# Kernel tuning notes

Hardware: AMD Instinct MI355X
Metric: run time of the kernel (lower is better)

Reference implementation:

```python
import jax, jax.numpy as jnp
import numpy as np

MAX_DEG = 3
DEG_DIMS = [1, 3, 5, 7]          # degree_to_dim(d) = 2d+1
SUM_DIM = 16                     # sum of DEG_DIMS
FREQ_SUM = 44                    # sum over (d_in,d_out) of 2*min(d_in,d_out)+1
C = 32                           # channels per degree (in == out, FULL fusion)
EDGE_DIM = 2                     # fiber_edge[0] + 1
MID = 32                         # RadialProfile mid_dim
E = 4096
N = 1024


def setup_inputs() -> dict:
    key = jax.random.key(0)
    ks = jax.random.split(key, 16)
    inp = {}
    for d, dim in enumerate(DEG_DIMS):
        inp[f"node_feats_{d}"] = jax.random.normal(ks[d], (N, C, dim), jnp.float32)
    inp["edge_feats_0"] = jax.random.normal(ks[4], (E, EDGE_DIM, 1), jnp.float32)
    inp["basis"] = jax.random.normal(ks[5], (E, SUM_DIM, FREQ_SUM, SUM_DIM), jnp.float32)
    inp["src"] = jax.random.randint(ks[6], (E,), 0, N, dtype=jnp.int32)
    inp["dst"] = jax.random.randint(ks[7], (E,), 0, N, dtype=jnp.int32)
    # RadialProfile params: Linear(2,32) -> ReLU -> Linear(32,32) -> ReLU -> Linear(32, 44*32*32, bias=False)
    inp["w1"] = jax.random.normal(ks[8], (EDGE_DIM, MID), jnp.float32) / np.sqrt(EDGE_DIM)
    inp["b1"] = jnp.zeros((MID,), jnp.float32)
    inp["w2"] = jax.random.normal(ks[9], (MID, MID), jnp.float32) / np.sqrt(MID)
    inp["b2"] = jnp.zeros((MID,), jnp.float32)
    inp["w3"] = jax.random.normal(ks[10], (MID, FREQ_SUM * C * C), jnp.float32) / np.sqrt(MID)
    # self-interaction kernels per output degree
    for d in range(MAX_DEG + 1):
        inp[f"kernel_self_{d}"] = jax.random.normal(ks[11 + d], (C, C), jnp.float32) / np.sqrt(C)
    return inp


def _conv_se3(node_feats, edge_feats_0, basis, src, dst,
              w1, b1, w2, b2, w3, kernels_self):
    e = edge_feats_0.shape[0]
    # invariant edge feats: [E, edge_dim]
    inv = edge_feats_0[..., 0]
    # gather source node features and fuse along representation dim: [E, C, 16]
    feats = jnp.concatenate([nf[src] for nf in node_feats], axis=-1)
    # RadialProfile MLP -> radial weights [E, C_out, C_in * FREQ_SUM]
    h = jax.nn.relu(inv @ w1 + b1)
    h = jax.nn.relu(h @ w2 + b2)
    radial_weights = (h @ w3).reshape(e, C, C * FREQ_SUM)
    # VersatileConvSE3 fused path:
    # tmp = (features @ basis_view).view(E, C*FREQ_SUM, SUM_DIM)
    basis_view = basis.reshape(e, SUM_DIM, FREQ_SUM * SUM_DIM)
    tmp = jnp.einsum('eci,eix->ecx', feats, basis_view).reshape(e, C * FREQ_SUM, SUM_DIM)
    out_fused = jnp.einsum('eok,eks->eos', radial_weights, tmp)  # [E, C, 16]
    # unfuse by degree, add self-interaction at dst, pool (copy_e_sum) to nodes
    outs = []
    off = 0
    for d, dim in enumerate(DEG_DIMS):
        o = out_fused[..., off:off + dim]
        o = o + jnp.einsum('oc,ecd->eod', kernels_self[d], node_feats[d][dst])
        outs.append(jax.ops.segment_sum(o, dst, num_segments=N))
        off += dim
    # return fused node output [N, C, 16] (concat of degrees 0..3)
    return jnp.concatenate(outs, axis=-1)


def reference(node_feats_0, node_feats_1, node_feats_2, node_feats_3,
              edge_feats_0, basis, src, dst,
              w1, b1, w2, b2, w3,
              kernel_self_0, kernel_self_1, kernel_self_2, kernel_self_3):
    return _conv_se3([node_feats_0, node_feats_1, node_feats_2, node_feats_3],
                     edge_feats_0, basis, src, dst,
                     w1, b1, w2, b2, w3,
                     [kernel_self_0, kernel_self_1, kernel_self_2, kernel_self_3])
```

## Files before the change

kernel.cpp:

```cpp
#include <hip/hip_runtime.h>
#include <hip/hip_bf16.h>

#define NN 1024
#define EE 4096
#define CC 32
#define SD 16
#define FQ 44
#define MIDC 32
#define EB 16

typedef short s16x4 __attribute__((ext_vector_type(4)));
typedef short s16x8 __attribute__((ext_vector_type(8)));
typedef float fx4 __attribute__((ext_vector_type(4)));

__device__ __forceinline__ unsigned short f2b(float x) {
    __hip_bfloat16 b = __float2bfloat16(x);
    return *reinterpret_cast<unsigned short*>(&b);
}

__global__ __launch_bounds__(256) void k_w3t2(const float* __restrict__ w3,
                                              unsigned short* __restrict__ w3t2) {
    int tid = blockIdx.x * 256 + threadIdx.x;
    int m = tid & 31;
    int o = (tid >> 5) & 31;
    int c = tid >> 10;
    const float* rp = &w3[(size_t)m * 45056 + o * 1408 + c * 44];
    float v[44];
#pragma unroll
    for (int q = 0; q < 11; q++) {
        float4 t4 = *(const float4*)(rp + q * 4);
        v[q * 4 + 0] = t4.x; v[q * 4 + 1] = t4.y;
        v[q * 4 + 2] = t4.z; v[q * 4 + 3] = t4.w;
    }
#pragma unroll
    for (int f = 0; f < FQ; f++) {
        w3t2[(((size_t)f * CC + o) * CC + c) * CC + m] = f2b(v[f]);
    }
}

__global__ __launch_bounds__(256) void k_h(const float* __restrict__ ef,
                                           const float* __restrict__ w1,
                                           const float* __restrict__ b1,
                                           const float* __restrict__ w2,
                                           const float* __restrict__ b2,
                                           const int* __restrict__ dst,
                                           unsigned short* __restrict__ h2,
                                           int* __restrict__ deg) {
    int e = blockIdx.x * 256 + threadIdx.x;
    if (e >= EE) return;
    float i0 = ef[e * 2 + 0], i1 = ef[e * 2 + 1];
    float h1[MIDC];
#pragma unroll
    for (int j = 0; j < MIDC; j++) {
        float v = i0 * w1[j] + i1 * w1[MIDC + j] + b1[j];
        h1[j] = v > 0.f ? v : 0.f;
    }
    for (int j = 0; j < MIDC; j++) {
        float v = b2[j];
#pragma unroll
        for (int m = 0; m < MIDC; m++) v += h1[m] * w2[m * MIDC + j];
        v = v > 0.f ? v : 0.f;
        h2[e * MIDC + j] = f2b(v);
    }
    atomicAdd(&deg[dst[e]], 1);
}

__global__ __launch_bounds__(512, 4) void k_main(
    const float* __restrict__ nf0, const float* __restrict__ nf1,
    const float* __restrict__ nf2, const float* __restrict__ nf3,
    const float* __restrict__ basis, const int* __restrict__ src,
    const int* __restrict__ dst, const unsigned short* __restrict__ h2,
    const unsigned short* __restrict__ w3t2, float* __restrict__ out) {
    __shared__ __align__(16) unsigned short rad_lds[EB * CC * CC];
    __shared__ __align__(16) unsigned short U_lds[EB * SD * 40];
    __shared__ __align__(16) unsigned short basT[EB * SD * 40];

    int t = threadIdx.x;
    int wave = t >> 6;
    int l = t & 63;
    int l15 = l & 15;
    int kg = l >> 4;
    int eg = blockIdx.x >> 1;
    int fhalf = blockIdx.x & 1;
    int eb = eg * EB;

    float* fstage = (float*)rad_lds;
    {
        int e = t >> 5, c = t & 31;
        int sn = src[eb + e];
        float* row = &fstage[(e * CC + c) * SD];
        row[0] = nf0[sn * CC + c];
#pragma unroll
        for (int j = 0; j < 3; j++) row[1 + j] = nf1[(sn * CC + c) * 3 + j];
#pragma unroll
        for (int j = 0; j < 5; j++) row[4 + j] = nf2[(sn * CC + c) * 5 + j];
#pragma unroll
        for (int j = 0; j < 7; j++) row[9 + j] = nf3[(sn * CC + c) * 7 + j];
    }
    s16x8 h2frag = *(const s16x8*)(h2 + ((size_t)(eb + l15) * MIDC + (kg << 3)));
    __syncthreads();

    s16x8 feats[2][2];
#pragma unroll
    for (int ei = 0; ei < 2; ei++) {
        int e = wave * 2 + ei;
#pragma unroll
        for (int ch = 0; ch < 2; ch++) {
            int cc = ch * 16 + l15;
            s16x8 fr = {};
            if (kg < 2) {
                const float4* fp4 = (const float4*)&fstage[(e * CC + cc) * SD + kg * 8];
                float4 a = fp4[0], b = fp4[1];
                fr[0] = (short)f2b(a.x); fr[1] = (short)f2b(a.y);
                fr[2] = (short)f2b(a.z); fr[3] = (short)f2b(a.w);
                fr[4] = (short)f2b(b.x); fr[5] = (short)f2b(b.y);
                fr[6] = (short)f2b(b.z); fr[7] = (short)f2b(b.w);
            }
            feats[ei][ch] = fr;
        }
    }
    for (int k = t; k < EB * SD * 40; k += 512) basT[k] = 0;
    __syncthreads();

    fx4 acc[4];
#pragma unroll
    for (int q = 0; q < 4; q++) acc[q] = (fx4){0.f, 0.f, 0.f, 0.f};
    fx4 zz = (fx4){0.f, 0.f, 0.f, 0.f};

    for (int fi = 0; fi < 22; fi++) {
        int f = fhalf * 22 + fi;

        {
            int e = t >> 5, i = (t >> 1) & 15, sh = t & 1;
            const float* gp = &basis[(((size_t)(eb + e) * SD + i) * FQ + f) * SD + sh * 8];
            float4 v0 = *(const float4*)gp;
            float4 v1 = *(const float4*)(gp + 4);
            float vs[8] = {v0.x, v0.y, v0.z, v0.w, v1.x, v1.y, v1.z, v1.w};
#pragma unroll
            for (int j = 0; j < 8; j++) {
                int s = sh * 8 + j;
                int byte = (e * SD + s) * 80 + i * 2;
                byte ^= ((((e & 1) << 1) | (s >> 3)) << 4);
                *(unsigned short*)((char*)basT + byte) = f2b(vs[j]);
            }
        }

#pragma unroll
        for (int j = 0; j < 8; j++) {
            int o = wave * 4 + (j >> 1);
            int ch = j & 1;
            const s16x8* ap = (const s16x8*)(w3t2 +
                ((((size_t)f * CC + o) * CC + ch * 16 + l15) * CC + (kg << 3)));
            s16x8 af = *ap;
            fx4 cf = __builtin_amdgcn_mfma_f32_16x16x32_bf16(af, h2frag, zz, 0, 0, 0);
            int c_w = ch * 16 + (kg << 2);
            int byte = l15 * 2048 + o * 64 + c_w * 2;
            byte ^= (((l15 ^ o) & 7) << 4);
            s16x4 pk;
            pk[0] = (short)f2b(cf[0]); pk[1] = (short)f2b(cf[1]);
            pk[2] = (short)f2b(cf[2]); pk[3] = (short)f2b(cf[3]);
            *(s16x4*)((char*)rad_lds + byte) = pk;
        }
        __syncthreads();

#pragma unroll
        for (int ei = 0; ei < 2; ei++) {
            int e = wave * 2 + ei;
            int bbyte = (e * SD + l15) * 80 + kg * 16;
            bbyte ^= ((((e & 1) << 1) | (l15 >> 3)) << 4);
            s16x8 bb = *(const s16x8*)((char*)basT + bbyte);
#pragma unroll
            for (int ch = 0; ch < 2; ch++) {
                fx4 u = __builtin_amdgcn_mfma_f32_16x16x32_bf16(feats[ei][ch], bb, zz, 0, 0, 0);
                int c_w = ch * 16 + (kg << 2);
                int ubyte = (e * SD + l15) * 80 + c_w * 2;
                s16x4 pk;
                pk[0] = (short)f2b(u[0]); pk[1] = (short)f2b(u[1]);
                pk[2] = (short)f2b(u[2]); pk[3] = (short)f2b(u[3]);
                *(s16x4*)((char*)U_lds + ubyte) = pk;
            }
            int ubyte2 = (e * SD + l15) * 80 + kg * 16;
            s16x8 ub = *(const s16x8*)((char*)U_lds + ubyte2);
#pragma unroll
            for (int oh = 0; oh < 2; oh++) {
                int o = oh * 16 + l15;
                int abyte = e * 2048 + o * 64 + kg * 16;
                abyte ^= (((e ^ o) & 7) << 4);
                s16x8 ra = *(const s16x8*)((char*)rad_lds + abyte);
                acc[ei * 2 + oh] =
                    __builtin_amdgcn_mfma_f32_16x16x32_bf16(ra, ub, acc[ei * 2 + oh], 0, 0, 0);
            }
        }
        __syncthreads();
    }

#pragma unroll
    for (int ei = 0; ei < 2; ei++) {
        int e = wave * 2 + ei;
        int d = dst[eb + e];
        float* op = &out[(size_t)d * (CC * SD)];
#pragma unroll
        for (int oh = 0; oh < 2; oh++) {
            fx4 a = acc[ei * 2 + oh];
#pragma unroll
            for (int r = 0; r < 4; r++) {
                int o = oh * 16 + (kg << 2) + r;
                atomicAdd(&op[o * SD + l15], a[r]);
            }
        }
    }
}

__global__ __launch_bounds__(256) void k_self(
    const float* __restrict__ nf0, const float* __restrict__ nf1,
    const float* __restrict__ nf2, const float* __restrict__ nf3,
    const float* __restrict__ ks0, const float* __restrict__ ks1,
    const float* __restrict__ ks2, const float* __restrict__ ks3,
    const int* __restrict__ deg, float* __restrict__ out) {
    int idx = blockIdx.x * 256 + threadIdx.x;
    if (idx >= NN * CC * SD) return;
    int n = idx >> 9;
    int rem = idx & 511;
    int o = rem >> 4;
    int s = rem & 15;
    const float* nf;
    const float* ks;
    int dim, off;
    if (s < 1) { nf = nf0; ks = ks0; dim = 1; off = 0; }
    else if (s < 4) { nf = nf1; ks = ks1; dim = 3; off = 1; }
    else if (s < 9) { nf = nf2; ks = ks2; dim = 5; off = 4; }
    else { nf = nf3; ks = ks3; dim = 7; off = 9; }
    int j = s - off;
    float acc = 0.f;
#pragma unroll
    for (int c = 0; c < CC; c++) acc += ks[o * CC + c] * nf[(n * CC + c) * dim + j];
    out[idx] += (float)deg[n] * acc;
}

extern "C" void kernel_launch(void* const* d_in, const int* in_sizes, int n_in,
                              void* d_out, int out_size, void* d_ws, size_t ws_size,
                              hipStream_t stream) {
    const float* nf0 = (const float*)d_in[0];
    const float* nf1 = (const float*)d_in[1];
    const float* nf2 = (const float*)d_in[2];
    const float* nf3 = (const float*)d_in[3];
    const float* ef = (const float*)d_in[4];
    const float* basis = (const float*)d_in[5];
    const int* src = (const int*)d_in[6];
    const int* dst = (const int*)d_in[7];
    const float* w1 = (const float*)d_in[8];
    const float* b1 = (const float*)d_in[9];
    const float* w2 = (const float*)d_in[10];
    const float* b2 = (const float*)d_in[11];
    const float* w3 = (const float*)d_in[12];
    const float* ks0 = (const float*)d_in[13];
    const float* ks1 = (const float*)d_in[14];
    const float* ks2 = (const float*)d_in[15];
    const float* ks3 = (const float*)d_in[16];
    float* out = (float*)d_out;

    unsigned short* h2 = (unsigned short*)d_ws;
    int* deg = (int*)((char*)d_ws + EE * MIDC * 2);
    unsigned short* w3t2 = (unsigned short*)((char*)d_ws + EE * MIDC * 2 + 4096);

    hipMemsetAsync(d_out, 0, (size_t)out_size * sizeof(float), stream);
    hipMemsetAsync(deg, 0, NN * sizeof(int), stream);

    k_w3t2<<<128, 256, 0, stream>>>(w3, w3t2);
    k_h<<<EE / 256, 256, 0, stream>>>(ef, w1, b1, w2, b2, dst, h2, deg);
    k_main<<<512, 512, 0, stream>>>(nf0, nf1, nf2, nf3, basis, src, dst, h2, w3t2, out);
    k_self<<<(NN * CC * SD) / 256, 256, 0, stream>>>(nf0, nf1, nf2, nf3, ks0, ks1,
                                                     ks2, ks3, deg, out);
}
```

Before: 130.9 us.

## Prefetch basis into registers one frequency ahead, skip basT LDS staging

Basis values for the next frequency are loaded straight into registers in the MFMA B-fragment layout and prefetched one iteration ahead, so the LDS transpose buffer (basT) and its zero-fill go away. The U scratch is now per-wave. The aim is to hide global basis load latency behind the radial MFMA work and to cut LDS traffic. The trade-offs are more live registers and strided 4-byte global loads in place of float4 loads, which may lower coalescing efficiency.

```diff
diff --git a/kernel.cpp b/kernel.cpp
--- a/kernel.cpp
+++ b/kernel.cpp
@@ -8,6 +8,8 @@
 #define FQ 44
 #define MIDC 32
 #define EB 16
+#define NFQ 2
+#define FPB 22
 
 typedef short s16x4 __attribute__((ext_vector_type(4)));
 typedef short s16x8 __attribute__((ext_vector_type(8)));
@@ -72,17 +74,17 @@
     const int* __restrict__ dst, const unsigned short* __restrict__ h2,
     const unsigned short* __restrict__ w3t2, float* __restrict__ out) {
     __shared__ __align__(16) unsigned short rad_lds[EB * CC * CC];
-    __shared__ __align__(16) unsigned short U_lds[EB * SD * 40];
-    __shared__ __align__(16) unsigned short basT[EB * SD * 40];
+    __shared__ __align__(16) unsigned short u_scr[16 * 640];
 
     int t = threadIdx.x;
-    int wave = t >> 6;
+    int wv = t >> 6;
     int l = t & 63;
     int l15 = l & 15;
     int kg = l >> 4;
     int eg = blockIdx.x >> 1;
-    int fhalf = blockIdx.x & 1;
+    int fq = blockIdx.x & 1;
     int eb = eg * EB;
+    int f0 = fq * FPB;
 
     float* fstage = (float*)rad_lds;
     {
@@ -103,13 +105,13 @@
     s16x8 feats[2][2];
 #pragma unroll
     for (int ei = 0; ei < 2; ei++) {
-        int e = wave * 2 + ei;
+        int e = (wv << 1) + ei;
 #pragma unroll
         for (int ch = 0; ch < 2; ch++) {
-            int cc = ch * 16 + l15;
             s16x8 fr = {};
             if (kg < 2) {
-                const float4* fp4 = (const float4*)&fstage[(e * CC + cc) * SD + kg * 8];
+                const float4* fp4 =
+                    (const float4*)&fstage[(e * CC + (ch << 4) + l15) * SD + (kg << 3)];
                 float4 a = fp4[0], b = fp4[1];
                 fr[0] = (short)f2b(a.x); fr[1] = (short)f2b(a.y);
                 fr[2] = (short)f2b(a.z); fr[3] = (short)f2b(a.w);
@@ -119,76 +121,91 @@
             feats[ei][ch] = fr;
         }
     }
-    for (int k = t; k < EB * SD * 40; k += 512) basT[k] = 0;
     __syncthreads();
 
-    fx4 acc[4];
-#pragma unroll
-    for (int q = 0; q < 4; q++) acc[q] = (fx4){0.f, 0.f, 0.f, 0.f};
+    fx4 acc[2][2];
+#pragma unroll
+    for (int q = 0; q < 4; q++) acc[q >> 1][q & 1] = (fx4){0.f, 0.f, 0.f, 0.f};
     fx4 zz = (fx4){0.f, 0.f, 0.f, 0.f};
 
-    for (int fi = 0; fi < 22; fi++) {
-        int f = fhalf * 22 + fi;
-
-        {
-            int e = t >> 5, i = (t >> 1) & 15, sh = t & 1;
-            const float* gp = &basis[(((size_t)(eb + e) * SD + i) * FQ + f) * SD + sh * 8];
-            float4 v0 = *(const float4*)gp;
-            float4 v1 = *(const float4*)(gp + 4);
-            float vs[8] = {v0.x, v0.y, v0.z, v0.w, v1.x, v1.y, v1.z, v1.w};
-#pragma unroll
-            for (int j = 0; j < 8; j++) {
-                int s = sh * 8 + j;
-                int byte = (e * SD + s) * 80 + i * 2;
-                byte ^= ((((e & 1) << 1) | (s >> 3)) << 4);
-                *(unsigned short*)((char*)basT + byte) = f2b(vs[j]);
-            }
-        }
+    float pf[2][8];
+#define ISSUE_PF(FNEXT)                                                                   \
+    if (kg < 2) {                                                                         \
+        _Pragma("unroll") for (int ei = 0; ei < 2; ei++) {                                \
+            int e_ = (wv << 1) + ei;                                                      \
+            const float* bp =                                                             \
+                &basis[(((size_t)(eb + e_) * SD + (kg << 3)) * FQ + (FNEXT)) * SD + l15]; \
+            _Pragma("unroll") for (int j = 0; j < 8; j++)                                 \
+                pf[ei][j] = bp[(size_t)j * (FQ * SD)];                                    \
+        }                                                                                 \
+    }
+
+    ISSUE_PF(f0);
+
+    s16x8 bb[2];
+
+    for (int fi = 0; fi < FPB; fi++) {
+        int f = f0 + fi;
 
 #pragma unroll
         for (int j = 0; j < 8; j++) {
-            int o = wave * 4 + (j >> 1);
+            int o = (wv << 2) + (j >> 1);
             int ch = j & 1;
-            const s16x8* ap = (const s16x8*)(w3t2 +
-                ((((size_t)f * CC + o) * CC + ch * 16 + l15) * CC + (kg << 3)));
-            s16x8 af = *ap;
+            s16x8 af = *(const s16x8*)(w3t2 +
+                ((((size_t)f * CC + o) * CC + (ch << 4) + l15) * CC + (kg << 3)));
             fx4 cf = __builtin_amdgcn_mfma_f32_16x16x32_bf16(af, h2frag, zz, 0, 0, 0);
-            int c_w = ch * 16 + (kg << 2);
-            int byte = l15 * 2048 + o * 64 + c_w * 2;
-            byte ^= (((l15 ^ o) & 7) << 4);
+            int byte = (l15 << 11) + (o << 6) + (ch << 5) + (kg << 3);
+            byte ^= ((l15 ^ o) & 7) << 4;
             s16x4 pk;
             pk[0] = (short)f2b(cf[0]); pk[1] = (short)f2b(cf[1]);
             pk[2] = (short)f2b(cf[2]); pk[3] = (short)f2b(cf[3]);
             *(s16x4*)((char*)rad_lds + byte) = pk;
         }
+
+#pragma unroll
+        for (int ei = 0; ei < 2; ei++) {
+            s16x8 b = {};
+            if (kg < 2) {
+#pragma unroll
+                for (int j = 0; j < 8; j++) b[j] = (short)f2b(pf[ei][j]);
+            }
+            bb[ei] = b;
+        }
         __syncthreads();
 
-#pragma unroll
-        for (int ei = 0; ei < 2; ei++) {
-            int e = wave * 2 + ei;
-            int bbyte = (e * SD + l15) * 80 + kg * 16;
-            bbyte ^= ((((e & 1) << 1) | (l15 >> 3)) << 4);
-            s16x8 bb = *(const s16x8*)((char*)basT + bbyte);
+        if (fi + 1 < FPB) { ISSUE_PF(f + 1); }
+
+        fx4 u[2][2];
+#pragma unroll
+        for (int ei = 0; ei < 2; ei++) {
+#pragma unroll
+            for (int ch = 0; ch < 2; ch++)
+                u[ei][ch] = __builtin_amdgcn_mfma_f32_16x16x32_bf16(feats[ei][ch], bb[ei], zz, 0, 0, 0);
+        }
+#pragma unroll
+        for (int ei = 0; ei < 2; ei++) {
+            int rbase = ((wv << 1) + ei) * 1280;
 #pragma unroll
             for (int ch = 0; ch < 2; ch++) {
-                fx4 u = __builtin_amdgcn_mfma_f32_16x16x32_bf16(feats[ei][ch], bb, zz, 0, 0, 0);
-                int c_w = ch * 16 + (kg << 2);
-                int ubyte = (e * SD + l15) * 80 + c_w * 2;
                 s16x4 pk;
-                pk[0] = (short)f2b(u[0]); pk[1] = (short)f2b(u[1]);
-                pk[2] = (short)f2b(u[2]); pk[3] = (short)f2b(u[3]);
-                *(s16x4*)((char*)U_lds + ubyte) = pk;
-            }
-            int ubyte2 = (e * SD + l15) * 80 + kg * 16;
-            s16x8 ub = *(const s16x8*)((char*)U_lds + ubyte2);
+                pk[0] = (short)f2b(u[ei][ch][0]); pk[1] = (short)f2b(u[ei][ch][1]);
+                pk[2] = (short)f2b(u[ei][ch][2]); pk[3] = (short)f2b(u[ei][ch][3]);
+                *(s16x4*)((char*)u_scr + rbase + l15 * 80 + (ch << 5) + (kg << 3)) = pk;
+            }
+        }
+#pragma unroll
+        for (int ei = 0; ei < 2; ei++) {
+            int e = (wv << 1) + ei;
+            int rbase = ((wv << 1) + ei) * 1280;
+            s16x8 ub = *(const s16x8*)((char*)u_scr + rbase + l15 * 80 + (kg << 4));
 #pragma unroll
             for (int oh = 0; oh < 2; oh++) {
-                int o = oh * 16 + l15;
-                int abyte = e * 2048 + o * 64 + kg * 16;
-                abyte ^= (((e ^ o) & 7) << 4);
+                int o = (oh << 4) + l15;
+                int abyte = (e << 11) + (o << 6) + (kg << 4);
+                abyte ^= ((e ^ o) & 7) << 4;
                 s16x8 ra = *(const s16x8*)((char*)rad_lds + abyte);
-                acc[ei * 2 + oh] =
-                    __builtin_amdgcn_mfma_f32_16x16x32_bf16(ra, ub, acc[ei * 2 + oh], 0, 0, 0);
+                acc[ei][oh] =
+                    __builtin_amdgcn_mfma_f32_16x16x32_bf16(ra, ub, acc[ei][oh], 0, 0, 0);
             }
         }
         __syncthreads();
@@ -196,16 +213,15 @@
 
 #pragma unroll
     for (int ei = 0; ei < 2; ei++) {
-        int e = wave * 2 + ei;
+        int e = (wv << 1) + ei;
         int d = dst[eb + e];
         float* op = &out[(size_t)d * (CC * SD)];
 #pragma unroll
         for (int oh = 0; oh < 2; oh++) {
-            fx4 a = acc[ei * 2 + oh];
 #pragma unroll
             for (int r = 0; r < 4; r++) {
-                int o = oh * 16 + (kg << 2) + r;
-                atomicAdd(&op[o * SD + l15], a[r]);
+                int o = (oh << 4) + (kg << 2) + r;
+                atomicAdd(&op[o * SD + l15], acc[ei][oh][r]);
             }
         }
     }
@@ -268,7 +284,8 @@
 
     k_w3t2<<<128, 256, 0, stream>>>(w3, w3t2);
     k_h<<<EE / 256, 256, 0, stream>>>(ef, w1, b1, w2, b2, dst, h2, deg);
-    k_main<<<512, 512, 0, stream>>>(nf0, nf1, nf2, nf3, basis, src, dst, h2, w3t2, out);
+    k_main<<<(EE / EB) * NFQ, 512, 0, stream>>>(nf0, nf1, nf2, nf3, basis, src, dst,
+                                                h2, w3t2, out);
     k_self<<<(NN * CC * SD) / 256, 256, 0, stream>>>(nf0, nf1, nf2, nf3, ks0, ks1,
                                                      ks2, ks3, deg, out);
 }
```

Measured after the change: 137.5 us. 1.05x slower.
